# Kernel optimization log

Measured on AMD Instinct MI355X. Metric: run time of the kernel, lower is better.

## Reference

```python
import jax, jax.numpy as jnp
import numpy as np

D_MODEL = 512
H = 8
D_K = D_MODEL // H


def setup_inputs() -> dict:
    key = jax.random.key(0)
    ks = jax.random.split(key, 11)
    B, S = 2, 4096
    scale = 1.0 / np.sqrt(D_MODEL)
    inp = {
        "q": jax.random.normal(ks[0], (B, S, D_MODEL), jnp.float32),
        "k": jax.random.normal(ks[1], (B, S, D_MODEL), jnp.float32),
        "v": jax.random.normal(ks[2], (B, S, D_MODEL), jnp.float32),
        "wq": jax.random.normal(ks[3], (D_MODEL, D_MODEL), jnp.float32) * scale,
        "bq": jnp.zeros((D_MODEL,), jnp.float32),
        "wk": jax.random.normal(ks[4], (D_MODEL, D_MODEL), jnp.float32) * scale,
        "bk": jnp.zeros((D_MODEL,), jnp.float32),
        "wv": jax.random.normal(ks[5], (D_MODEL, D_MODEL), jnp.float32) * scale,
        "bv": jnp.zeros((D_MODEL,), jnp.float32),
        "wo": jax.random.normal(ks[6], (D_MODEL, D_MODEL), jnp.float32) * scale,
        "bo": jnp.zeros((D_MODEL,), jnp.float32),
    }
    return inp


def reference(q, k, v, wq, bq, wk, bk, wv, bv, wo, bo):
    B, S, _ = q.shape
    # Linear projections (torch Linear: x @ W.T + b), split into heads -> [B,H,S,Dk]
    def proj(x, w, b):
        y = jnp.einsum('bsd,ed->bse', x, w) + b
        return y.reshape(B, -1, H, D_K).transpose(0, 2, 1, 3)

    qh = proj(q, wq, bq)
    kh = proj(k, wk, bk)
    vh = proj(v, wv, bv)

    # scaled dot-product attention, full [B,H,S,S] scores (faithful to source)
    scores = jnp.einsum('bhqd,bhkd->bhqk', qh, kh) / jnp.sqrt(jnp.asarray(D_K, qh.dtype))
    attn = jax.nn.softmax(scores, axis=-1)
    x = jnp.einsum('bhqk,bhkd->bhqd', attn, vh)

    # merge heads and output projection
    x = x.transpose(0, 2, 1, 3).reshape(B, S, H * D_K)
    return jnp.einsum('bsd,ed->bse', x, wo) + bo
```

## Files before the change

kernel.cpp:

```cpp
#include <hip/hip_runtime.h>

#define DM 512
#define NH 8
#define DK 64
#define SEQ 4096

typedef short bf16x8 __attribute__((ext_vector_type(8)));
typedef float f32x4 __attribute__((ext_vector_type(4)));
typedef unsigned short u16;
typedef u16 u16x8 __attribute__((ext_vector_type(8)));
typedef u16 u16x4 __attribute__((ext_vector_type(4)));
typedef unsigned int u32;
typedef u32 u32x2 __attribute__((ext_vector_type(2)));

__device__ __forceinline__ u16 f2bf(float f) {
  union { float f; unsigned u; } v; v.f = f;
  unsigned r = v.u + 0x7fffu + ((v.u >> 16) & 1u);
  return (u16)(r >> 16);
}

__device__ __forceinline__ u32 cvtpk(float a, float b) {
  u32 r; asm("v_cvt_pk_bf16_f32 %0, %1, %2" : "=v"(r) : "v"(a), "v"(b)); return r;
}

__device__ __forceinline__ float fexp2(float x) {
  float r; asm("v_exp_f32 %0, %1" : "=v"(r) : "v"(x)); return r;
}

__device__ __forceinline__ float fmax3(float a, float b, float c) {
  return fmaxf(fmaxf(a, b), c);
}

__global__ __launch_bounds__(256, 2)
void gemm_qkv(const float* __restrict__ qx, const float* __restrict__ kx,
              const float* __restrict__ vx,
              const float* __restrict__ wq, const float* __restrict__ bq,
              const float* __restrict__ wk, const float* __restrict__ bk,
              const float* __restrict__ wv, const float* __restrict__ bv,
              u16* __restrict__ Qh, u16* __restrict__ Kh, u16* __restrict__ Vt)
{
  __shared__ alignas(16) u16 Alds[64][72];
  __shared__ alignas(16) u16 Blds[128][72];
  const int mode = blockIdx.x >> 9;
  const int bid = blockIdx.x & 511;
  const float* X = (mode == 0) ? qx : (mode == 1) ? kx : vx;
  const float* W = (mode == 0) ? wq : (mode == 1) ? wk : wv;
  const float* Bs = (mode == 0) ? bq : (mode == 1) ? bk : bv;

  const int t = threadIdx.x;
  const int bx = bid & 127, by = bid >> 7;
  const int m0 = bx << 6, n0 = by << 7;
  const int lane = t & 63, w = t >> 6;
  const int lr = lane & 15, lg = lane >> 4;
  const int wr = w >> 1, wc = w & 1;

  f32x4 acc[2][4];
  #pragma unroll
  for (int i = 0; i < 2; ++i)
    #pragma unroll
    for (int j = 0; j < 4; ++j) acc[i][j] = (f32x4){0.f, 0.f, 0.f, 0.f};

  float4 xa[4]; float4 wb[8];
  auto loadX = [&](int k0) {
    #pragma unroll
    for (int i = 0; i < 4; ++i) {
      int f = (i << 8) + t;
      xa[i] = *(const float4*)(X + (size_t)(m0 + (f >> 4)) * 512 + k0 + ((f & 15) << 2));
    }
    #pragma unroll
    for (int i = 0; i < 8; ++i) {
      int f = (i << 8) + t;
      wb[i] = *(const float4*)(W + (size_t)(n0 + (f >> 4)) * 512 + k0 + ((f & 15) << 2));
    }
  };

  loadX(0);
  for (int k0 = 0; k0 < 512; k0 += 64) {
    __syncthreads();
    #pragma unroll
    for (int i = 0; i < 4; ++i) {
      int f = (i << 8) + t;
      u16x4 p = { f2bf(xa[i].x), f2bf(xa[i].y), f2bf(xa[i].z), f2bf(xa[i].w) };
      *(u16x4*)&Alds[f >> 4][(f & 15) << 2] = p;
    }
    #pragma unroll
    for (int i = 0; i < 8; ++i) {
      int f = (i << 8) + t;
      u16x4 p = { f2bf(wb[i].x), f2bf(wb[i].y), f2bf(wb[i].z), f2bf(wb[i].w) };
      *(u16x4*)&Blds[f >> 4][(f & 15) << 2] = p;
    }
    __syncthreads();
    if (k0 + 64 < 512) loadX(k0 + 64);

    #pragma unroll
    for (int kk = 0; kk < 2; ++kk) {
      bf16x8 af[2], bfr[4];
      #pragma unroll
      for (int mi = 0; mi < 2; ++mi)
        af[mi] = *(const bf16x8*)&Alds[(wr << 5) + (mi << 4) + lr][(kk << 5) + (lg << 3)];
      #pragma unroll
      for (int ni = 0; ni < 4; ++ni)
        bfr[ni] = *(const bf16x8*)&Blds[(wc << 6) + (ni << 4) + lr][(kk << 5) + (lg << 3)];
      #pragma unroll
      for (int mi = 0; mi < 2; ++mi)
        #pragma unroll
        for (int ni = 0; ni < 4; ++ni)
          acc[mi][ni] = __builtin_amdgcn_mfma_f32_16x16x32_bf16(af[mi], bfr[ni], acc[mi][ni], 0, 0, 0);
    }
  }

  const float sc = (mode == 0) ? 0.18033688f : 1.0f;
  #pragma unroll
  for (int mi = 0; mi < 2; ++mi) {
    #pragma unroll
    for (int ni = 0; ni < 4; ++ni) {
      const int e = n0 + (wc << 6) + (ni << 4) + lr;
      const int m = m0 + (wr << 5) + (mi << 4) + (lg << 2);
      const float bb = Bs[e];
      const int b = m >> 12, s = m & 4095, h = e >> 6, dk = e & 63;
      if (mode != 2) {
        u16* O = (mode == 0) ? Qh : Kh;
        size_t base = ((size_t)((b << 3) + h) * SEQ + s) * DK + dk;
        #pragma unroll
        for (int r = 0; r < 4; ++r)
          O[base + (size_t)r * DK] = f2bf((acc[mi][ni][r] + bb) * sc);
      } else {
        size_t base = ((size_t)((b << 3) + h) * DK + dk) * SEQ + s;
        u16x4 p = { f2bf(acc[mi][ni][0] + bb), f2bf(acc[mi][ni][1] + bb),
                    f2bf(acc[mi][ni][2] + bb), f2bf(acc[mi][ni][3] + bb) };
        *(u16x4*)(Vt + base) = p;
      }
    }
  }
}

__global__ __launch_bounds__(256, 2)
void gemm_out(const u16* __restrict__ Xa, const float* __restrict__ W,
              const float* __restrict__ bias, float* __restrict__ Out)
{
  __shared__ alignas(16) u16 Alds[64][72];
  __shared__ alignas(16) u16 Blds[128][72];
  const int t = threadIdx.x;
  const int bx = blockIdx.x & 127, by = blockIdx.x >> 7;
  const int m0 = bx << 6, n0 = by << 7;
  const int lane = t & 63, w = t >> 6;
  const int lr = lane & 15, lg = lane >> 4;
  const int wr = w >> 1, wc = w & 1;

  f32x4 acc[2][4];
  #pragma unroll
  for (int i = 0; i < 2; ++i)
    #pragma unroll
    for (int j = 0; j < 4; ++j) acc[i][j] = (f32x4){0.f, 0.f, 0.f, 0.f};

  u16x8 xa3[2]; float4 wb[8];
  auto loadX = [&](int k0) {
    #pragma unroll
    for (int i = 0; i < 2; ++i) {
      int f = (i << 8) + t;
      xa3[i] = *(const u16x8*)(Xa + (size_t)(m0 + (f >> 3)) * 512 + k0 + ((f & 7) << 3));
    }
    #pragma unroll
    for (int i = 0; i < 8; ++i) {
      int f = (i << 8) + t;
      wb[i] = *(const float4*)(W + (size_t)(n0 + (f >> 4)) * 512 + k0 + ((f & 15) << 2));
    }
  };

  loadX(0);
  for (int k0 = 0; k0 < 512; k0 += 64) {
    __syncthreads();
    #pragma unroll
    for (int i = 0; i < 2; ++i) {
      int f = (i << 8) + t;
      *(u16x8*)&Alds[f >> 3][(f & 7) << 3] = xa3[i];
    }
    #pragma unroll
    for (int i = 0; i < 8; ++i) {
      int f = (i << 8) + t;
      u16x4 p = { f2bf(wb[i].x), f2bf(wb[i].y), f2bf(wb[i].z), f2bf(wb[i].w) };
      *(u16x4*)&Blds[f >> 4][(f & 15) << 2] = p;
    }
    __syncthreads();
    if (k0 + 64 < 512) loadX(k0 + 64);

    #pragma unroll
    for (int kk = 0; kk < 2; ++kk) {
      bf16x8 af[2], bfr[4];
      #pragma unroll
      for (int mi = 0; mi < 2; ++mi)
        af[mi] = *(const bf16x8*)&Alds[(wr << 5) + (mi << 4) + lr][(kk << 5) + (lg << 3)];
      #pragma unroll
      for (int ni = 0; ni < 4; ++ni)
        bfr[ni] = *(const bf16x8*)&Blds[(wc << 6) + (ni << 4) + lr][(kk << 5) + (lg << 3)];
      #pragma unroll
      for (int mi = 0; mi < 2; ++mi)
        #pragma unroll
        for (int ni = 0; ni < 4; ++ni)
          acc[mi][ni] = __builtin_amdgcn_mfma_f32_16x16x32_bf16(af[mi], bfr[ni], acc[mi][ni], 0, 0, 0);
    }
  }

  #pragma unroll
  for (int mi = 0; mi < 2; ++mi) {
    #pragma unroll
    for (int ni = 0; ni < 4; ++ni) {
      const int e = n0 + (wc << 6) + (ni << 4) + lr;
      const int m = m0 + (wr << 5) + (mi << 4) + (lg << 2);
      const float bb = bias[e];
      size_t base = (size_t)m * 512 + e;
      #pragma unroll
      for (int r = 0; r < 4; ++r) Out[base + (size_t)r * 512] = acc[mi][ni][r] + bb;
    }
  }
}

__global__ __launch_bounds__(256, 2)
void attn_kernel(const u16* __restrict__ Qh, const u16* __restrict__ Kh,
                 const u16* __restrict__ Vt, u16* __restrict__ Xa)
{
  __shared__ alignas(16) u16 smem[33792];

  const int t = threadIdx.x;
  const int lane = t & 63, w = t >> 6;
  const int lr = lane & 15, lg = lane >> 4;
  const int ob = ((blockIdx.x & 7) << 6) + (blockIdx.x >> 3);
  const int qb = ob & 31, bh = ob >> 5;
  const size_t qkbase = (size_t)bh * SEQ * DK;
  const size_t vbase  = (size_t)bh * DK * SEQ;
  u16* P0 = smem + 16384 + w * 4352;
  u16* P1 = P0 + 2176;

  bf16x8 qf[2][2];
  #pragma unroll
  for (int mi = 0; mi < 2; ++mi)
    #pragma unroll
    for (int kk = 0; kk < 2; ++kk) {
      int qrow = (qb << 7) + (w << 5) + (mi << 4) + lr;
      qf[mi][kk] = *(const bf16x8*)(Qh + qkbase + (size_t)qrow * DK + (kk << 5) + (lg << 3));
    }

  bf16x8 onesf;
  {
    u16 one = (lr == 0) ? (u16)0x3F80 : (u16)0;
    #pragma unroll
    for (int j = 0; j < 8; ++j) onesf[j] = (short)one;
  }

  float mrun[2] = {-3e38f, -3e38f};
  f32x4 o[2][4], osum[2];
  #pragma unroll
  for (int mi = 0; mi < 2; ++mi) {
    #pragma unroll
    for (int dt = 0; dt < 4; ++dt) o[mi][dt] = (f32x4){0.f, 0.f, 0.f, 0.f};
    osum[mi] = (f32x4){0.f, 0.f, 0.f, 0.f};
  }

  const u16* Kg = Kh + qkbase;
  const u16* Vg = Vt + vbase;
  int kro[4], kco[4], kdst[4], vro[4], vco[4], vdst[4];
  #pragma unroll
  for (int i = 0; i < 4; ++i) {
    int G = t + (i << 8);
    int kr = G >> 3, kc = G & 7;
    int vr = G >> 4, vc = G & 15;
    kro[i] = kr; kco[i] = kc << 3;
    vro[i] = vr; vco[i] = vc << 3;
    kdst[i] = kr * 64 + ((kc ^ (kr & 7)) << 3);
    vdst[i] = 8192 + vr * 128 + ((vc ^ (vr & 15)) << 3);
  }

  u16x8 kpr[4], vpr[4];
  #pragma unroll
  for (int i = 0; i < 4; ++i) {
    kpr[i] = *(const u16x8*)(Kg + (size_t)kro[i] * 64 + kco[i]);
    vpr[i] = *(const u16x8*)(Vg + (size_t)vro[i] * SEQ + vco[i]);
  }

  auto softmax_store = [&](f32x4* s, float& mr, f32x4* oo, f32x4& os, u16* P) {
    float tm[8];
    #pragma unroll
    for (int nt = 0; nt < 8; ++nt)
      tm[nt] = fmaxf(fmax3(s[nt][0], s[nt][1], s[nt][2]), s[nt][3]);
    float tmax = fmax3(fmax3(tm[0], tm[1], tm[2]), fmax3(tm[3], tm[4], tm[5]),
                       fmaxf(tm[6], tm[7]));
    tmax = fmaxf(tmax, __shfl_xor(tmax, 16));
    tmax = fmaxf(tmax, __shfl_xor(tmax, 32));
    if (!__all(tmax <= mr + 8.f)) {
      float mnew = fmaxf(mr, tmax);
      float scl = fexp2(mr - mnew);
      mr = mnew;
      os[0] *= scl;
      #pragma unroll
      for (int dt = 0; dt < 4; ++dt) oo[dt] *= scl;
    }
    const float mm = mr;
    #pragma unroll
    for (int nt = 0; nt < 8; ++nt) {
      float e0 = fexp2(s[nt][0] - mm), e1 = fexp2(s[nt][1] - mm);
      float e2 = fexp2(s[nt][2] - mm), e3 = fexp2(s[nt][3] - mm);
      u32x2 pk2 = { cvtpk(e0, e1), cvtpk(e2, e3) };
      *(u32x2*)((char*)P + lr * 272 + (nt << 5) + (lg << 3)) = pk2;
    }
  };

  for (int it = 0; it < SEQ / 128; ++it) {
    __syncthreads();
    #pragma unroll
    for (int i = 0; i < 4; ++i) {
      *(u16x8*)&smem[kdst[i]] = kpr[i];
      *(u16x8*)&smem[vdst[i]] = vpr[i];
    }
    __syncthreads();
    if (it + 1 < SEQ / 128) {
      const int kv0n = (it + 1) << 7;
      #pragma unroll
      for (int i = 0; i < 4; ++i) {
        kpr[i] = *(const u16x8*)(Kg + (size_t)(kv0n + kro[i]) * 64 + kco[i]);
        vpr[i] = *(const u16x8*)(Vg + (size_t)vro[i] * SEQ + kv0n + vco[i]);
      }
    }

    f32x4 s0[8], s1[8];
    #pragma unroll
    for (int nt = 0; nt < 8; ++nt) {
      s0[nt] = (f32x4){0.f, 0.f, 0.f, 0.f};
      s1[nt] = (f32x4){0.f, 0.f, 0.f, 0.f};
    }
    #pragma unroll
    for (int nt = 0; nt < 8; ++nt) {
      const int row = ((nt << 4) + lr) * 64;
      bf16x8 kf0 = *(const bf16x8*)&smem[row + ((lg ^ (lr & 7)) << 3)];
      bf16x8 kf1 = *(const bf16x8*)&smem[row + (((4 + lg) ^ (lr & 7)) << 3)];
      __builtin_amdgcn_s_setprio(1);
      s0[nt] = __builtin_amdgcn_mfma_f32_16x16x32_bf16(kf0, qf[0][0], s0[nt], 0, 0, 0);
      s0[nt] = __builtin_amdgcn_mfma_f32_16x16x32_bf16(kf1, qf[0][1], s0[nt], 0, 0, 0);
      s1[nt] = __builtin_amdgcn_mfma_f32_16x16x32_bf16(kf0, qf[1][0], s1[nt], 0, 0, 0);
      s1[nt] = __builtin_amdgcn_mfma_f32_16x16x32_bf16(kf1, qf[1][1], s1[nt], 0, 0, 0);
      __builtin_amdgcn_s_setprio(0);
    }

    softmax_store(s0, mrun[0], o[0], osum[0], P0);
    softmax_store(s1, mrun[1], o[1], osum[1], P1);

    #pragma unroll
    for (int kk = 0; kk < 4; ++kk) {
      bf16x8 vf[4];
      #pragma unroll
      for (int dt = 0; dt < 4; ++dt)
        vf[dt] = *(const bf16x8*)&smem[8192 + ((dt << 4) + lr) * 128 +
                                       ((((kk << 2) + lg) ^ lr) << 3)];
      bf16x8 pf0 = *(const bf16x8*)&P0[lr * 136 + (kk << 5) + (lg << 3)];
      bf16x8 pf1 = *(const bf16x8*)&P1[lr * 136 + (kk << 5) + (lg << 3)];
      __builtin_amdgcn_s_setprio(1);
      #pragma unroll
      for (int dt = 0; dt < 4; ++dt)
        o[0][dt] = __builtin_amdgcn_mfma_f32_16x16x32_bf16(vf[dt], pf0, o[0][dt], 0, 0, 0);
      osum[0] = __builtin_amdgcn_mfma_f32_16x16x32_bf16(onesf, pf0, osum[0], 0, 0, 0);
      #pragma unroll
      for (int dt = 0; dt < 4; ++dt)
        o[1][dt] = __builtin_amdgcn_mfma_f32_16x16x32_bf16(vf[dt], pf1, o[1][dt], 0, 0, 0);
      osum[1] = __builtin_amdgcn_mfma_f32_16x16x32_bf16(onesf, pf1, osum[1], 0, 0, 0);
      __builtin_amdgcn_s_setprio(0);
    }
  }
  __syncthreads();

  #pragma unroll
  for (int mi = 0; mi < 2; ++mi) {
    float lsum = __shfl(osum[mi][0], lr);
    float inv = 1.f / lsum;
    #pragma unroll
    for (int dt = 0; dt < 4; ++dt) {
      u16x4 v4 = { f2bf(o[mi][dt][0] * inv), f2bf(o[mi][dt][1] * inv),
                   f2bf(o[mi][dt][2] * inv), f2bf(o[mi][dt][3] * inv) };
      int row = (w << 5) + (mi << 4) + lr;
      *(u16x4*)&smem[row * 72 + (dt << 4) + (lg << 2)] = v4;
    }
  }
  __syncthreads();
  {
    const int b = bh >> 3, h = bh & 7;
    #pragma unroll
    for (int i = 0; i < 4; ++i) {
      int f = (i << 8) + t;
      int row = f >> 3, c8 = (f & 7) << 3;
      u16x8 val = *(const u16x8*)&smem[row * 72 + c8];
      *(u16x8*)(Xa + ((size_t)b * SEQ + (qb << 7) + row) * DM + (h << 6) + c8) = val;
    }
  }
}

extern "C" void kernel_launch(void* const* d_in, const int* in_sizes, int n_in,
                              void* d_out, int out_size, void* d_ws, size_t ws_size,
                              hipStream_t stream)
{
  const float* q  = (const float*)d_in[0];
  const float* k  = (const float*)d_in[1];
  const float* v  = (const float*)d_in[2];
  const float* wq = (const float*)d_in[3];
  const float* bq = (const float*)d_in[4];
  const float* wk = (const float*)d_in[5];
  const float* bk = (const float*)d_in[6];
  const float* wv = (const float*)d_in[7];
  const float* bv = (const float*)d_in[8];
  const float* wo = (const float*)d_in[9];
  const float* bo = (const float*)d_in[10];

  const size_t HS = (size_t)2 * NH * SEQ * DK;
  u16* Qh = (u16*)d_ws;
  u16* Kh = Qh + HS;
  u16* Vt = Kh + HS;
  u16* Xa = Vt + HS;

  gemm_qkv<<<1536, 256, 0, stream>>>(q, k, v, wq, bq, wk, bk, wv, bv, Qh, Kh, Vt);
  attn_kernel<<<512, 256, 0, stream>>>(Qh, Kh, Vt, Xa);
  gemm_out<<<512, 256, 0, stream>>>(Xa, wo, bo, (float*)d_out);
}
```

Measured before the change: 150.0 us.

## Halve KV tile to 64, shrink LDS, process query subtiles sequentially

Cuts the attention KV tile from 128 to 64 keys and shrinks shared memory from about 66KB to 25KB, so more blocks can be resident per CU. K and V fragments are loaded into registers once per tile and reused by both query subtiles, which now run one after another through a single per-wave P buffer. The softmax computes exponentials before the lazy-rescale check and starts the running max at 0 instead of a large negative value. In exchange there are twice as many barrier-separated iterations, and the first-tile exponentials can overflow if a score exceeds roughly 128 in log2 units.

```diff
diff --git a/kernel.cpp b/kernel.cpp
--- a/kernel.cpp
+++ b/kernel.cpp
@@ -219,7 +219,7 @@
 void attn_kernel(const u16* __restrict__ Qh, const u16* __restrict__ Kh,
                  const u16* __restrict__ Vt, u16* __restrict__ Xa)
 {
-  __shared__ alignas(16) u16 smem[33792];
+  __shared__ alignas(16) u16 smem[12800];
 
   const int t = threadIdx.x;
   const int lane = t & 63, w = t >> 6;
@@ -228,8 +228,7 @@
   const int qb = ob & 31, bh = ob >> 5;
   const size_t qkbase = (size_t)bh * SEQ * DK;
   const size_t vbase  = (size_t)bh * DK * SEQ;
-  u16* P0 = smem + 16384 + w * 4352;
-  u16* P1 = P0 + 2176;
+  u16* Pw = smem + 8192 + w * 1152;
 
   bf16x8 qf[2][2];
   #pragma unroll
@@ -247,7 +246,7 @@
     for (int j = 0; j < 8; ++j) onesf[j] = (short)one;
   }
 
-  float mrun[2] = {-3e38f, -3e38f};
+  float mrun[2] = {0.f, 0.f};
   f32x4 o[2][4], osum[2];
   #pragma unroll
   for (int mi = 0; mi < 2; ++mi) {
@@ -258,110 +257,100 @@
 
   const u16* Kg = Kh + qkbase;
   const u16* Vg = Vt + vbase;
-  int kro[4], kco[4], kdst[4], vro[4], vco[4], vdst[4];
-  #pragma unroll
-  for (int i = 0; i < 4; ++i) {
-    int G = t + (i << 8);
-    int kr = G >> 3, kc = G & 7;
-    int vr = G >> 4, vc = G & 15;
-    kro[i] = kr; kco[i] = kc << 3;
-    vro[i] = vr; vco[i] = vc << 3;
-    kdst[i] = kr * 64 + ((kc ^ (kr & 7)) << 3);
-    vdst[i] = 8192 + vr * 128 + ((vc ^ (vr & 15)) << 3);
-  }
-
-  u16x8 kpr[4], vpr[4];
-  #pragma unroll
-  for (int i = 0; i < 4; ++i) {
-    kpr[i] = *(const u16x8*)(Kg + (size_t)kro[i] * 64 + kco[i]);
-    vpr[i] = *(const u16x8*)(Vg + (size_t)vro[i] * SEQ + vco[i]);
-  }
-
-  auto softmax_store = [&](f32x4* s, float& mr, f32x4* oo, f32x4& os, u16* P) {
-    float tm[8];
-    #pragma unroll
-    for (int nt = 0; nt < 8; ++nt)
-      tm[nt] = fmaxf(fmax3(s[nt][0], s[nt][1], s[nt][2]), s[nt][3]);
-    float tmax = fmax3(fmax3(tm[0], tm[1], tm[2]), fmax3(tm[3], tm[4], tm[5]),
-                       fmaxf(tm[6], tm[7]));
-    tmax = fmaxf(tmax, __shfl_xor(tmax, 16));
-    tmax = fmaxf(tmax, __shfl_xor(tmax, 32));
-    if (!__all(tmax <= mr + 8.f)) {
-      float mnew = fmaxf(mr, tmax);
-      float scl = fexp2(mr - mnew);
-      mr = mnew;
-      os[0] *= scl;
-      #pragma unroll
-      for (int dt = 0; dt < 4; ++dt) oo[dt] *= scl;
-    }
-    const float mm = mr;
-    #pragma unroll
-    for (int nt = 0; nt < 8; ++nt) {
-      float e0 = fexp2(s[nt][0] - mm), e1 = fexp2(s[nt][1] - mm);
-      float e2 = fexp2(s[nt][2] - mm), e3 = fexp2(s[nt][3] - mm);
-      u32x2 pk2 = { cvtpk(e0, e1), cvtpk(e2, e3) };
-      *(u32x2*)((char*)P + lr * 272 + (nt << 5) + (lg << 3)) = pk2;
-    }
-  };
-
-  for (int it = 0; it < SEQ / 128; ++it) {
-    __syncthreads();
-    #pragma unroll
-    for (int i = 0; i < 4; ++i) {
-      *(u16x8*)&smem[kdst[i]] = kpr[i];
-      *(u16x8*)&smem[vdst[i]] = vpr[i];
-    }
-    __syncthreads();
-    if (it + 1 < SEQ / 128) {
-      const int kv0n = (it + 1) << 7;
-      #pragma unroll
-      for (int i = 0; i < 4; ++i) {
-        kpr[i] = *(const u16x8*)(Kg + (size_t)(kv0n + kro[i]) * 64 + kco[i]);
-        vpr[i] = *(const u16x8*)(Vg + (size_t)vro[i] * SEQ + kv0n + vco[i]);
-      }
-    }
-
-    f32x4 s0[8], s1[8];
-    #pragma unroll
-    for (int nt = 0; nt < 8; ++nt) {
-      s0[nt] = (f32x4){0.f, 0.f, 0.f, 0.f};
-      s1[nt] = (f32x4){0.f, 0.f, 0.f, 0.f};
-    }
-    #pragma unroll
-    for (int nt = 0; nt < 8; ++nt) {
-      const int row = ((nt << 4) + lr) * 64;
-      bf16x8 kf0 = *(const bf16x8*)&smem[row + ((lg ^ (lr & 7)) << 3)];
-      bf16x8 kf1 = *(const bf16x8*)&smem[row + (((4 + lg) ^ (lr & 7)) << 3)];
+  const int r0 = t >> 3, c0 = t & 7;
+  const int r1 = r0 + 32, c1 = c0;
+  const int wk0 = r0 * 64 + ((c0 ^ (r0 & 7)) << 3);
+  const int wk1 = r1 * 64 + ((c1 ^ (r1 & 7)) << 3);
+
+  u16x8 kr0, kr1, vr0, vr1;
+  kr0 = *(const u16x8*)(Kg + (size_t)r0 * 64 + (c0 << 3));
+  kr1 = *(const u16x8*)(Kg + (size_t)r1 * 64 + (c1 << 3));
+  vr0 = *(const u16x8*)(Vg + (size_t)r0 * SEQ + (c0 << 3));
+  vr1 = *(const u16x8*)(Vg + (size_t)r1 * SEQ + (c1 << 3));
+
+  for (int it = 0; it < SEQ / 64; ++it) {
+    __syncthreads();
+    *(u16x8*)&smem[wk0]        = kr0;
+    *(u16x8*)&smem[wk1]        = kr1;
+    *(u16x8*)&smem[4096 + wk0] = vr0;
+    *(u16x8*)&smem[4096 + wk1] = vr1;
+    __syncthreads();
+    if (it + 1 < SEQ / 64) {
+      const int kv0n = (it + 1) << 6;
+      kr0 = *(const u16x8*)(Kg + (size_t)(kv0n + r0) * 64 + (c0 << 3));
+      kr1 = *(const u16x8*)(Kg + (size_t)(kv0n + r1) * 64 + (c1 << 3));
+      vr0 = *(const u16x8*)(Vg + (size_t)r0 * SEQ + kv0n + (c0 << 3));
+      vr1 = *(const u16x8*)(Vg + (size_t)r1 * SEQ + kv0n + (c1 << 3));
+    }
+
+    bf16x8 kf[4][2], vf[4][2];
+    #pragma unroll
+    for (int nt = 0; nt < 4; ++nt)
+      #pragma unroll
+      for (int kk = 0; kk < 2; ++kk) {
+        const int off = ((nt << 4) + lr) * 64 + ((((kk << 2) + lg) ^ (lr & 7)) << 3);
+        kf[nt][kk] = *(const bf16x8*)&smem[off];
+        vf[nt][kk] = *(const bf16x8*)&smem[4096 + off];
+      }
+
+    #pragma unroll
+    for (int mi = 0; mi < 2; ++mi) {
+      f32x4 s[4];
+      #pragma unroll
+      for (int nt = 0; nt < 4; ++nt) s[nt] = (f32x4){0.f, 0.f, 0.f, 0.f};
       __builtin_amdgcn_s_setprio(1);
-      s0[nt] = __builtin_amdgcn_mfma_f32_16x16x32_bf16(kf0, qf[0][0], s0[nt], 0, 0, 0);
-      s0[nt] = __builtin_amdgcn_mfma_f32_16x16x32_bf16(kf1, qf[0][1], s0[nt], 0, 0, 0);
-      s1[nt] = __builtin_amdgcn_mfma_f32_16x16x32_bf16(kf0, qf[1][0], s1[nt], 0, 0, 0);
-      s1[nt] = __builtin_amdgcn_mfma_f32_16x16x32_bf16(kf1, qf[1][1], s1[nt], 0, 0, 0);
+      #pragma unroll
+      for (int kk = 0; kk < 2; ++kk)
+        #pragma unroll
+        for (int nt = 0; nt < 4; ++nt)
+          s[nt] = __builtin_amdgcn_mfma_f32_16x16x32_bf16(kf[nt][kk], qf[mi][kk], s[nt], 0, 0, 0);
       __builtin_amdgcn_s_setprio(0);
-    }
-
-    softmax_store(s0, mrun[0], o[0], osum[0], P0);
-    softmax_store(s1, mrun[1], o[1], osum[1], P1);
-
-    #pragma unroll
-    for (int kk = 0; kk < 4; ++kk) {
-      bf16x8 vf[4];
-      #pragma unroll
-      for (int dt = 0; dt < 4; ++dt)
-        vf[dt] = *(const bf16x8*)&smem[8192 + ((dt << 4) + lr) * 128 +
-                                       ((((kk << 2) + lg) ^ lr) << 3)];
-      bf16x8 pf0 = *(const bf16x8*)&P0[lr * 136 + (kk << 5) + (lg << 3)];
-      bf16x8 pf1 = *(const bf16x8*)&P1[lr * 136 + (kk << 5) + (lg << 3)];
-      __builtin_amdgcn_s_setprio(1);
-      #pragma unroll
-      for (int dt = 0; dt < 4; ++dt)
-        o[0][dt] = __builtin_amdgcn_mfma_f32_16x16x32_bf16(vf[dt], pf0, o[0][dt], 0, 0, 0);
-      osum[0] = __builtin_amdgcn_mfma_f32_16x16x32_bf16(onesf, pf0, osum[0], 0, 0, 0);
-      #pragma unroll
-      for (int dt = 0; dt < 4; ++dt)
-        o[1][dt] = __builtin_amdgcn_mfma_f32_16x16x32_bf16(vf[dt], pf1, o[1][dt], 0, 0, 0);
-      osum[1] = __builtin_amdgcn_mfma_f32_16x16x32_bf16(onesf, pf1, osum[1], 0, 0, 0);
-      __builtin_amdgcn_s_setprio(0);
+
+      float m0 = fmax3(s[0][0], s[0][1], s[0][2]);
+      float m1 = fmax3(s[0][3], s[1][0], s[1][1]);
+      float m2 = fmax3(s[1][2], s[1][3], s[2][0]);
+      float m3 = fmax3(s[2][1], s[2][2], s[2][3]);
+      float m4 = fmax3(s[3][0], s[3][1], s[3][2]);
+      float tmax = fmaxf(fmax3(m0, m1, m2), fmax3(m3, m4, s[3][3]));
+      tmax = fmaxf(tmax, __shfl_xor(tmax, 16));
+      tmax = fmaxf(tmax, __shfl_xor(tmax, 32));
+
+      const float mm = mrun[mi];
+      #pragma unroll
+      for (int nt = 0; nt < 4; ++nt) {
+        s[nt][0] = fexp2(s[nt][0] - mm);
+        s[nt][1] = fexp2(s[nt][1] - mm);
+        s[nt][2] = fexp2(s[nt][2] - mm);
+        s[nt][3] = fexp2(s[nt][3] - mm);
+      }
+
+      if (!__all(tmax <= mm + 8.f)) {
+        float mnew = fmaxf(mm, tmax);
+        float f = fexp2(mm - mnew);
+        mrun[mi] = mnew;
+        osum[mi][0] *= f;
+        #pragma unroll
+        for (int dt = 0; dt < 4; ++dt) o[mi][dt] *= f;
+        #pragma unroll
+        for (int nt = 0; nt < 4; ++nt) s[nt] *= f;
+      }
+
+      #pragma unroll
+      for (int nt = 0; nt < 4; ++nt) {
+        u32x2 pk2 = { cvtpk(s[nt][0], s[nt][1]), cvtpk(s[nt][2], s[nt][3]) };
+        *(u32x2*)((char*)Pw + lr * 144 + (nt << 5) + (lg << 3)) = pk2;
+      }
+
+      #pragma unroll
+      for (int kk = 0; kk < 2; ++kk) {
+        bf16x8 pf = *(const bf16x8*)&Pw[lr * 72 + (kk << 5) + (lg << 3)];
+        __builtin_amdgcn_s_setprio(1);
+        #pragma unroll
+        for (int dt = 0; dt < 4; ++dt)
+          o[mi][dt] = __builtin_amdgcn_mfma_f32_16x16x32_bf16(vf[dt][kk], pf, o[mi][dt], 0, 0, 0);
+        osum[mi] = __builtin_amdgcn_mfma_f32_16x16x32_bf16(onesf, pf, osum[mi], 0, 0, 0);
+        __builtin_amdgcn_s_setprio(0);
+      }
     }
   }
   __syncthreads();
```

New measurement: 150.9 us. No clear change (+0.6%).
